# Performance work log

Hardware: AMD Instinct MI355X
Metric: run time of the kernel (lower is better)

The kernel has to match this reference:

```python
import jax, jax.numpy as jnp
import numpy as np

B, H, W, C = 2, 64, 64, 256
G, K, L = 16, 9, 2
Cg = C // G


def _ln(x, g, b, eps=1e-6):
    m = jnp.mean(x, -1, keepdims=True)
    v = jnp.mean((x - m) ** 2, -1, keepdims=True)
    return (x - m) * jax.lax.rsqrt(v + eps) * g + b


def _conv(x, w, b=None, groups=1):
    y = jax.lax.conv_general_dilated(x, w, (1, 1), 'SAME',
        dimension_numbers=('NHWC', 'HWIO', 'NHWC'), feature_group_count=groups)
    return y if b is None else y + b


def _gelu(x):
    return jax.nn.gelu(x, approximate=False)  # torch nn.GELU (exact erf)


def _dcnv3(x, dw_w, dw_b, dwn_g, dwn_b, off_w, off_b, msk_w, msk_b,
           inp_w, inp_b, out_w, out_b, offset_scale=1.0):
    # x: [B,H,W,C] channels-last. kernel=3, stride=1, pad=1, dilation=1.
    xp = x @ inp_w + inp_b                                   # input_proj
    f = _gelu(_ln(_conv(x, dw_w, dw_b, groups=C), dwn_g, dwn_b))  # dw_conv branch
    off = (f @ off_w + off_b).reshape(B, H, W, G, K, 2) * offset_scale  # pixel units (x,y)
    mask = jax.nn.softmax((f @ msk_w + msk_b).reshape(B, H, W, G, K), axis=-1)
    dy, dx = jnp.meshgrid(jnp.arange(3.0) - 1.0, jnp.arange(3.0) - 1.0, indexing='ij')
    gx = dx.reshape(-1)
    gy = dy.reshape(-1)  # [K] kernel dilation grid
    # sampling locations in the zero-padded (pad=1) frame; pixel i center = i+0.5
    loc_x = (jnp.arange(W, dtype=x.dtype) + 1.5)[None, None, :, None, None] + gx + off[..., 0]
    loc_y = (jnp.arange(H, dtype=x.dtype) + 1.5)[None, :, None, None, None] + gy + off[..., 1]
    xg = jnp.pad(xp, ((0, 0), (1, 1), (1, 1), (0, 0))).reshape(B, H + 2, W + 2, G, Cg)
    px = loc_x - 0.5
    py = loc_y - 0.5
    x0 = jnp.floor(px).astype(jnp.int32)
    y0 = jnp.floor(py).astype(jnp.int32)
    fx = (px - x0)[..., None]
    fy = (py - y0)[..., None]
    Hp, Wp = H + 2, W + 2
    bi = jnp.arange(B).reshape(B, 1, 1, 1, 1)
    gi = jnp.arange(G).reshape(1, 1, 1, G, 1)

    def gather(yi, xi):  # zero padding outside bounds (grid_sample padding_mode='zeros')
        ok = ((yi >= 0) & (yi < Hp) & (xi >= 0) & (xi < Wp)).astype(x.dtype)[..., None]
        return xg[bi, jnp.clip(yi, 0, Hp - 1), jnp.clip(xi, 0, Wp - 1), gi] * ok

    top = gather(y0, x0) * (1 - fx) + gather(y0, x0 + 1) * fx
    bot = gather(y0 + 1, x0) * (1 - fx) + gather(y0 + 1, x0 + 1) * fx
    samp = top * (1 - fy) + bot * fy                         # [B,H,W,G,K,Cg]
    out = (samp * mask[..., None]).sum(4).reshape(B, H, W, C)
    return out @ out_w + out_b                               # output_proj


def _leffn(x, dc_w, dc_b, g, b, c1_w, c1_b, c2_w, c2_b, gamma):
    y = _ln(_conv(x, dc_w, dc_b, groups=C), g, b)
    y = _gelu(y @ c1_w + c1_b) @ c2_w + c2_b
    return x + gamma * y


def _cbam(x, w1, w2, sa_w, g, b):
    fc = lambda v: jax.nn.relu(v @ w1) @ w2
    ca = jax.nn.sigmoid(fc(x.mean((1, 2))) + fc(x.max((1, 2))))[:, None, None, :]
    x = x * ca
    sm = jnp.stack([x.mean(-1), x.max(-1)], -1)              # [B,H,W,2]
    x = x * jax.nn.sigmoid(_conv(sm, sa_w))
    return _ln(x, g, b)


def _upsample(x, w, bb, g, bt):
    y = jax.image.resize(x, (B, 2 * H, 2 * W, C), 'bilinear')  # align_corners=False
    y = _conv(y, w, bb)                                        # 3x3, C -> C//2
    return _gelu(_ln(y, g, bt))


def _forward(x, ln1_g, ln1_b, dw_w, dw_b, dwn_g, dwn_b, off_w, off_b, msk_w, msk_b,
             inp_w, inp_b, out_w, out_b, ln2_g, ln2_b, dc_w, dc_b, fn_g, fn_b,
             c1_w, c1_b, c2_w, c2_b, ffn_gamma, ca_w1, ca_w2, sa_w, cb_g, cb_b,
             nf_g, nf_b, up_w, up_b, up_g, up_bt):
    x = _cbam(x, ca_w1, ca_w2, sa_w, cb_g, cb_b)
    for i in range(L):  # fixed small depth; structural loop
        x = x + _dcnv3(_ln(x, ln1_g[i], ln1_b[i]), dw_w[i], dw_b[i], dwn_g[i], dwn_b[i],
                       off_w[i], off_b[i], msk_w[i], msk_b[i], inp_w[i], inp_b[i],
                       out_w[i], out_b[i])
        x = x + _leffn(_ln(x, ln2_g[i], ln2_b[i]), dc_w[i], dc_b[i], fn_g[i], fn_b[i],
                       c1_w[i], c1_b[i], c2_w[i], c2_b[i], ffn_gamma[i])
    x = _ln(x, nf_g, nf_b)
    return _upsample(x, up_w, up_b, up_g, up_bt)


def setup_inputs() -> dict:
    ks = iter(jax.random.split(jax.random.key(0), 80))
    r = lambda shp, s=0.02: jax.random.normal(next(ks), shp, dtype=jnp.float32) * s
    one = lambda shp: jnp.ones(shp, jnp.float32)
    zero = lambda shp: jnp.zeros(shp, jnp.float32)
    return dict(
        x=jax.random.normal(next(ks), (B, H, W, C), dtype=jnp.float32),
        ln1_g=one((L, C)), ln1_b=zero((L, C)),
        dw_w=r((L, 3, 3, 1, C)), dw_b=zero((L, C)),
        dwn_g=one((L, C)), dwn_b=zero((L, C)),
        off_w=r((L, C, G * K * 2), 0.01), off_b=zero((L, G * K * 2)),
        msk_w=r((L, C, G * K)), msk_b=zero((L, G * K)),
        inp_w=r((L, C, C)), inp_b=zero((L, C)),
        out_w=r((L, C, C)), out_b=zero((L, C)),
        ln2_g=one((L, C)), ln2_b=zero((L, C)),
        dc_w=r((L, 7, 7, 1, C)), dc_b=zero((L, C)),
        fn_g=one((L, C)), fn_b=zero((L, C)),
        c1_w=r((L, C, 4 * C)), c1_b=zero((L, 4 * C)),
        c2_w=r((L, 4 * C, C)), c2_b=zero((L, C)),
        ffn_gamma=0.7 * one((L, C)),
        ca_w1=r((C, C // 16)), ca_w2=r((C // 16, C)),
        sa_w=r((7, 7, 2, 1)),
        cb_g=one((C,)), cb_b=zero((C,)),
        nf_g=one((C,)), nf_b=zero((C,)),
        up_w=r((3, 3, C, C // 2)), up_b=zero((C // 2,)),
        up_g=one((C // 2,)), up_bt=zero((C // 2,)),
    )


def reference(x, ln1_g, ln1_b, dw_w, dw_b, dwn_g, dwn_b, off_w, off_b, msk_w, msk_b,
              inp_w, inp_b, out_w, out_b, ln2_g, ln2_b, dc_w, dc_b, fn_g, fn_b,
              c1_w, c1_b, c2_w, c2_b, ffn_gamma, ca_w1, ca_w2, sa_w, cb_g, cb_b,
              nf_g, nf_b, up_w, up_b, up_g, up_bt):
    return _forward(x, ln1_g, ln1_b, dw_w, dw_b, dwn_g, dwn_b, off_w, off_b, msk_w, msk_b,
                    inp_w, inp_b, out_w, out_b, ln2_g, ln2_b, dc_w, dc_b, fn_g, fn_b,
                    c1_w, c1_b, c2_w, c2_b, ffn_gamma, ca_w1, ca_w2, sa_w, cb_g, cb_b,
                    nf_g, nf_b, up_w, up_b, up_g, up_bt)
```

## Files before the change

kernel.cpp:

```cpp
#include <hip/hip_runtime.h>
#include <math.h>

#define B_ 2
#define H_ 64
#define W_ 64
#define C_ 256
#define G_ 16
#define HW_ (H_*W_)
#define M_ (B_*HW_)
#define C4_ (4*C_)
#define OFFN_ 288
#define MSKN_ 144
#define OMN_ 432
#define UH_ 128
#define UW_ 128
#define MUP_ (B_*UH_*UW_)
#define KUP_ (9*C_)
#define NOUT_ 128

typedef short short8 __attribute__((ext_vector_type(8)));
typedef float f32x4 __attribute__((ext_vector_type(4)));
typedef unsigned short us4 __attribute__((ext_vector_type(4)));

__device__ __forceinline__ float gelu_f(float x){
  return 0.5f * x * (1.f + erff(x * 0.70710678118654752440f));
}
__device__ __forceinline__ float sigmoid_f(float x){ return 1.f/(1.f+expf(-x)); }
__device__ __forceinline__ unsigned short f2bf(float x){
  unsigned int u = __float_as_uint(x);
  unsigned int r = (u + 0x7fffu + ((u>>16)&1u)) >> 16;
  return (unsigned short)r;
}
__device__ __forceinline__ float bf2f(unsigned short u){
  return __uint_as_float(((unsigned int)u) << 16);
}
__device__ __forceinline__ float bfl(unsigned int u){ return __uint_as_float(u<<16); }
__device__ __forceinline__ float bfh(unsigned int u){ return __uint_as_float(u & 0xffff0000u); }
__device__ __forceinline__ unsigned int pk(float a, float b){
  return (unsigned int)f2bf(a) | ((unsigned int)f2bf(b) << 16);
}

__device__ __forceinline__ void block_sum2(float& s, float& ss, float* sm){
  #pragma unroll
  for (int off=32; off>0; off>>=1){ s += __shfl_down(s, off); ss += __shfl_down(ss, off); }
  int lane = threadIdx.x & 63, wid = threadIdx.x >> 6;
  if (lane == 0){ sm[wid] = s; sm[4+wid] = ss; }
  __syncthreads();
  float a = 0.f, b = 0.f;
  int nw = blockDim.x >> 6;
  for (int i=0;i<nw;i++){ a += sm[i]; b += sm[4+i]; }
  s = a; ss = b;
}

__device__ __forceinline__ void block_summax(float& s, float& m, float* sm){
  #pragma unroll
  for (int off=32; off>0; off>>=1){ s += __shfl_down(s, off); m = fmaxf(m, __shfl_down(m, off)); }
  int lane = threadIdx.x & 63, wid = threadIdx.x >> 6;
  if (lane == 0){ sm[wid] = s; sm[4+wid] = m; }
  __syncthreads();
  float a = 0.f, b = -3.4e38f;
  int nw = blockDim.x >> 6;
  for (int i=0;i<nw;i++){ a += sm[i]; b = fmaxf(b, sm[4+i]); }
  s = a; m = b;
}

#define NJOBS 13
struct WtJobs {
  const float* src[NJOBS];
  unsigned short* dst[NJOBS];
  int Kd[NJOBS], Nd[NJOBS];
  int tOff[NJOBS+1];
};

__global__ __launch_bounds__(256) void k_wt_all(WtJobs J){
  __shared__ float tile[32][33];
  int bid = blockIdx.x;
  int j = 0;
  while (bid >= J.tOff[j+1]) j++;
  int lt = bid - J.tOff[j];
  const float* W = J.src[j];
  unsigned short* Wt = J.dst[j];
  int Kd = J.Kd[j], Nd = J.Nd[j];
  int ktiles = Kd >> 5;
  int k0 = (lt % ktiles) * 32, n0 = (lt / ktiles) * 32;
  int t = threadIdx.x;
  int r = t>>3, c4 = (t&7)*4;
  float4 v = make_float4(0.f,0.f,0.f,0.f);
  if (n0 + c4 < Nd) v = *(const float4*)(W + (size_t)(k0+r)*Nd + n0 + c4);
  tile[c4+0][r]=v.x; tile[c4+1][r]=v.y; tile[c4+2][r]=v.z; tile[c4+3][r]=v.w;
  __syncthreads();
  if (n0 + r < Nd){
    us4 o;
    o.x = f2bf(tile[r][c4+0]); o.y = f2bf(tile[r][c4+1]);
    o.z = f2bf(tile[r][c4+2]); o.w = f2bf(tile[r][c4+3]);
    *(us4*)(Wt + (size_t)(n0+r)*Kd + k0 + c4) = o;
  }
}

__global__ __launch_bounds__(256) void k_chpool(const float* __restrict__ Xin,
      float* __restrict__ psum, float* __restrict__ pmax){
  int chunk = blockIdx.x, b = blockIdx.y; int c = threadIdx.x;
  const float* p = Xin + (((size_t)b*HW_) + chunk*32)*C_ + c;
  float s = 0.f, m = -3.4e38f;
  for (int i=0;i<32;i++){ float v = p[(size_t)i*C_]; s += v; m = fmaxf(m, v); }
  psum[(b*128+chunk)*C_+c] = s; pmax[(b*128+chunk)*C_+c] = m;
}

__global__ __launch_bounds__(512) void k_ca(const float* __restrict__ psum, const float* __restrict__ pmax,
    const float* __restrict__ w1, const float* __restrict__ w2, float* __restrict__ ca){
  __shared__ float pm[2][256], px[2][256], hh[2][2][16];
  int t = threadIdx.x;
  {
    int b = t >> 8, c = t & 255;
    float s = 0.f, m = -3.4e38f;
    for (int ch=0; ch<128; ch++){ s += psum[(b*128+ch)*256+c]; m = fmaxf(m, pmax[(b*128+ch)*256+c]); }
    pm[b][c] = s * (1.f/4096.f); px[b][c] = m;
  }
  __syncthreads();
  if (t < 64){
    int b = t >> 5, typ = (t >> 4) & 1, j = t & 15;
    const float* src = typ ? px[b] : pm[b];
    float a = 0.f;
    for (int c2=0;c2<256;c2++) a += src[c2]*w1[c2*16+j];
    hh[b][typ][j] = fmaxf(a, 0.f);
  }
  __syncthreads();
  {
    int b = t >> 8, c = t & 255;
    float a = 0.f;
    for (int j=0;j<16;j++) a += (hh[b][0][j]+hh[b][1][j]) * w2[j*256+c];
    ca[b*256+c] = sigmoid_f(a);
  }
}

__global__ __launch_bounds__(256) void k_apply_ca(const float* __restrict__ Xin, float* __restrict__ X,
    const float* __restrict__ ca, float* __restrict__ smean, float* __restrict__ smax){
  __shared__ float sm[12];
  int pix = blockIdx.x, c = threadIdx.x;
  int b = pix >> 12;
  float v = Xin[(size_t)pix*C_+c] * ca[b*C_+c];
  X[(size_t)pix*C_+c] = v;
  float s = v, m = v;
  block_summax(s, m, sm);
  if (c == 0){ smean[pix] = s * (1.f/C_); smax[pix] = m; }
}

__global__ __launch_bounds__(256) void k_sa(const float* __restrict__ smean, const float* __restrict__ smax,
    const float* __restrict__ w, float* __restrict__ sa){
  int pix = blockIdx.x*256 + threadIdx.x;
  if (pix >= M_) return;
  int b = pix >> 12, hw = pix & 4095, h = hw >> 6, ww = hw & 63;
  float s = 0.f;
  for (int ky=0;ky<7;ky++){
    int hh = h + ky - 3; if (hh < 0 || hh >= H_) continue;
    for (int kx=0;kx<7;kx++){
      int xx = ww + kx - 3; if (xx < 0 || xx >= W_) continue;
      int q = (b<<12) + (hh<<6) + xx;
      s += smean[q]*w[(ky*7+kx)*2+0] + smax[q]*w[(ky*7+kx)*2+1];
    }
  }
  sa[pix] = sigmoid_f(s);
}

__global__ __launch_bounds__(256) void k_mul_ln_ln1(float* __restrict__ X, const float* __restrict__ sa,
    const float* __restrict__ g, const float* __restrict__ b,
    const float* __restrict__ g1, const float* __restrict__ b1, unsigned short* __restrict__ Tb){
  __shared__ float sm[12];
  int pix = blockIdx.x, c = threadIdx.x;
  float v = X[(size_t)pix*C_+c] * sa[pix];
  float s = v, ss = v*v;
  block_sum2(s, ss, sm);
  float mean = s * (1.f/C_), var = ss*(1.f/C_) - mean*mean;
  float r = rsqrtf(var + 1e-6f);
  float x0 = (v-mean)*r*g[c] + b[c];
  X[(size_t)pix*C_+c] = x0;
  __syncthreads();
  s = x0; ss = x0*x0;
  block_sum2(s, ss, sm);
  mean = s * (1.f/C_); var = ss*(1.f/C_) - mean*mean;
  r = rsqrtf(var + 1e-6f);
  Tb[(size_t)pix*C_+c] = f2bf((x0-mean)*r*g1[c] + b1[c]);
}

template<int KS, int DOGELU>
__global__ __launch_bounds__(256) void k_dwconv(const unsigned short* __restrict__ T,
    unsigned short* __restrict__ Out,
    const float* __restrict__ w, const float* __restrict__ bias,
    const float* __restrict__ g, const float* __restrict__ bb){
  constexpr int R = KS/2;
  int t = blockIdx.x*256 + threadIdx.x;
  int pix = t >> 5, grp = t & 31;
  int c0 = grp*8;
  int b = pix >> 12, hw = pix & 4095, h = hw >> 6, ww = hw & 63;
  float acc[8];
  {
    float4 b0 = *(const float4*)(bias + c0), b1 = *(const float4*)(bias + c0 + 4);
    acc[0]=b0.x; acc[1]=b0.y; acc[2]=b0.z; acc[3]=b0.w;
    acc[4]=b1.x; acc[5]=b1.y; acc[6]=b1.z; acc[7]=b1.w;
  }
  const unsigned short* tb = T + ((size_t)b*HW_)*C_ + c0;
  for (int ky=0;ky<KS;ky++){
    int hh = h + ky - R; if (hh < 0 || hh >= H_) continue;
    for (int kx=0;kx<KS;kx++){
      int xx = ww + kx - R; if (xx < 0 || xx >= W_) continue;
      uint4 a = *(const uint4*)(tb + ((size_t)hh*W_+xx)*C_);
      const float* wp = w + (ky*KS+kx)*C_ + c0;
      float4 w0 = *(const float4*)wp, w1 = *(const float4*)(wp+4);
      acc[0] += bfl(a.x)*w0.x; acc[1] += bfh(a.x)*w0.y;
      acc[2] += bfl(a.y)*w0.z; acc[3] += bfh(a.y)*w0.w;
      acc[4] += bfl(a.z)*w1.x; acc[5] += bfh(a.z)*w1.y;
      acc[6] += bfl(a.w)*w1.z; acc[7] += bfh(a.w)*w1.w;
    }
  }
  float s = 0.f, ss = 0.f;
  #pragma unroll
  for (int i=0;i<8;i++){ s += acc[i]; ss += acc[i]*acc[i]; }
  #pragma unroll
  for (int off=1; off<32; off<<=1){ s += __shfl_xor(s, off); ss += __shfl_xor(ss, off); }
  float mean = s * (1.f/C_), var = ss*(1.f/C_) - mean*mean;
  float r = rsqrtf(var + 1e-6f);
  float4 g0 = *(const float4*)(g + c0), g1 = *(const float4*)(g + c0 + 4);
  float4 p0 = *(const float4*)(bb + c0), p1 = *(const float4*)(bb + c0 + 4);
  float o[8];
  o[0]=(acc[0]-mean)*r*g0.x+p0.x; o[1]=(acc[1]-mean)*r*g0.y+p0.y;
  o[2]=(acc[2]-mean)*r*g0.z+p0.z; o[3]=(acc[3]-mean)*r*g0.w+p0.w;
  o[4]=(acc[4]-mean)*r*g1.x+p1.x; o[5]=(acc[5]-mean)*r*g1.y+p1.y;
  o[6]=(acc[6]-mean)*r*g1.z+p1.z; o[7]=(acc[7]-mean)*r*g1.w+p1.w;
  if (DOGELU){
    #pragma unroll
    for (int i=0;i<8;i++) o[i] = gelu_f(o[i]);
  }
  uint4 ov;
  ov.x = pk(o[0],o[1]); ov.y = pk(o[2],o[3]); ov.z = pk(o[4],o[5]); ov.w = pk(o[6],o[7]);
  *(uint4*)(Out + (size_t)pix*C_ + c0) = ov;
}

template<int TM, int EP, int OUTBF>
__global__ __launch_bounds__(256) void k_gemm_mfma(
    const unsigned short* __restrict__ A, const unsigned short* __restrict__ Bt,
    void* __restrict__ OutV, const float* __restrict__ bias,
    const float* __restrict__ bias2, int Ni, int Ki)
{
  constexpr int LD = 40;
  __shared__ unsigned short As[TM*LD];
  __shared__ unsigned short Bs[128*LD];
  const int tid = threadIdx.x;
  const int wave = tid >> 6, lane = tid & 63;
  const int m0 = blockIdx.x * TM, n0 = blockIdx.y * 128;
  const int wm0 = (wave >> 1) * (TM/2);
  const int wn0 = (wave & 1) * 64;
  constexpr int MI = TM/32;
  f32x4 acc[MI][4] = {};
  const int lm = lane & 15, kq = lane >> 4;
  constexpr int ACH = TM*4/256;

  for (int k0 = 0; k0 < Ki; k0 += 32){
    #pragma unroll
    for (int i=0;i<ACH;i++){
      int ch = tid*ACH + i;
      int r = ch >> 2, cc = (ch & 3) << 3;
      short8 v = *(const short8*)(A + (size_t)(m0 + r)*Ki + k0 + cc);
      *(short8*)(As + r*LD + cc) = v;
    }
    #pragma unroll
    for (int i=0;i<2;i++){
      int ch = tid + 256*i;
      int r = ch >> 2, cc = (ch & 3) << 3;
      short8 v = {};
      if (n0 + r < Ni) v = *(const short8*)(Bt + (size_t)(n0 + r)*Ki + k0 + cc);
      *(short8*)(Bs + r*LD + cc) = v;
    }
    __syncthreads();
    short8 af[MI], bf[4];
    #pragma unroll
    for (int mi=0;mi<MI;mi++) af[mi] = *(const short8*)(As + (wm0 + mi*16 + lm)*LD + kq*8);
    #pragma unroll
    for (int ni=0;ni<4;ni++)  bf[ni] = *(const short8*)(Bs + (wn0 + ni*16 + lm)*LD + kq*8);
    #pragma unroll
    for (int mi=0;mi<MI;mi++)
      #pragma unroll
      for (int ni=0;ni<4;ni++)
        acc[mi][ni] = __builtin_amdgcn_mfma_f32_16x16x32_bf16(af[mi], bf[ni], acc[mi][ni], 0,0,0);
    __syncthreads();
  }
  #pragma unroll
  for (int mi=0;mi<MI;mi++){
    #pragma unroll
    for (int ni=0;ni<4;ni++){
      int n = n0 + wn0 + ni*16 + lm;
      if (n < Ni){
        float bv;
        if constexpr (EP==4) bv = (n < OFFN_) ? bias[n] : bias2[n-OFFN_];
        else bv = bias[n];
        #pragma unroll
        for (int r=0;r<4;r++){
          int m = m0 + wm0 + mi*16 + kq*4 + r;
          size_t o = (size_t)m*Ni + n;
          float v = acc[mi][ni][r] + bv;
          if constexpr (EP==1) v = gelu_f(v);
          if constexpr (OUTBF) ((unsigned short*)OutV)[o] = f2bf(v);
          else                 ((float*)OutV)[o] = v;
        }
      }
    }
  }
}

template<int EP>
__global__ __launch_bounds__(256) void k_gemm_ln(
    const unsigned short* __restrict__ A, const unsigned short* __restrict__ Bt,
    float* __restrict__ X, const float* __restrict__ bias,
    const unsigned short* __restrict__ res2b, const float* __restrict__ gamma,
    unsigned short* __restrict__ OutTb,
    const float* __restrict__ lng, const float* __restrict__ lnb, int Ki)
{
  constexpr int LD = 40;
  __shared__ unsigned short As[32*LD];
  __shared__ unsigned short Bs[256*LD];
  __shared__ float rs[32][2], rq[32][2];
  const int tid = threadIdx.x;
  const int wave = tid >> 6, lane = tid & 63;
  const int m0 = blockIdx.x * 32;
  const int wm0 = (wave >> 1) * 16;
  const int wn0 = (wave & 1) * 128;
  const int lm = lane & 15, kq = lane >> 4;
  f32x4 acc[8] = {};

  for (int k0 = 0; k0 < Ki; k0 += 32){
    if (tid < 128){
      int r = tid >> 2, cc = (tid & 3) << 3;
      short8 v = *(const short8*)(A + (size_t)(m0 + r)*Ki + k0 + cc);
      *(short8*)(As + r*LD + cc) = v;
    }
    #pragma unroll
    for (int i=0;i<4;i++){
      int ch = tid + 256*i;
      int r = ch >> 2, cc = (ch & 3) << 3;
      short8 v = *(const short8*)(Bt + (size_t)r*Ki + k0 + cc);
      *(short8*)(Bs + r*LD + cc) = v;
    }
    __syncthreads();
    short8 af = *(const short8*)(As + (wm0 + lm)*LD + kq*8);
    short8 bf[8];
    #pragma unroll
    for (int ni=0;ni<8;ni++) bf[ni] = *(const short8*)(Bs + (wn0 + ni*16 + lm)*LD + kq*8);
    #pragma unroll
    for (int ni=0;ni<8;ni++)
      acc[ni] = __builtin_amdgcn_mfma_f32_16x16x32_bf16(af, bf[ni], acc[ni], 0,0,0);
    __syncthreads();
  }
  int nn[8]; float bv[8], gv[8];
  #pragma unroll
  for (int ni=0;ni<8;ni++){
    nn[ni] = wn0 + ni*16 + lm;
    bv[ni] = bias[nn[ni]];
    if constexpr (EP==3) gv[ni] = gamma[nn[ni]];
  }
  float ps[4] = {}, pq[4] = {};
  #pragma unroll
  for (int r=0;r<4;r++){
    int m = m0 + wm0 + kq*4 + r;
    #pragma unroll
    for (int ni=0;ni<8;ni++){
      size_t o = (size_t)m*C_ + nn[ni];
      float v = acc[ni][r] + bv[ni];
      if constexpr (EP==2) v = X[o] + v;
      if constexpr (EP==3) v = X[o] + bf2f(res2b[o]) + gv[ni]*v;
      X[o] = v;
      acc[ni][r] = v;
      ps[r] += v; pq[r] += v*v;
    }
  }
  #pragma unroll
  for (int off=1; off<16; off<<=1){
    #pragma unroll
    for (int r=0;r<4;r++){ ps[r] += __shfl_xor(ps[r], off); pq[r] += __shfl_xor(pq[r], off); }
  }
  if (lm == 0){
    #pragma unroll
    for (int r=0;r<4;r++){
      rs[wm0 + kq*4 + r][wave & 1] = ps[r];
      rq[wm0 + kq*4 + r][wave & 1] = pq[r];
    }
  }
  __syncthreads();
  float lg[8], lb[8];
  #pragma unroll
  for (int ni=0;ni<8;ni++){ lg[ni] = lng[nn[ni]]; lb[ni] = lnb[nn[ni]]; }
  #pragma unroll
  for (int r=0;r<4;r++){
    int row = wm0 + kq*4 + r;
    int m = m0 + row;
    float s = rs[row][0] + rs[row][1];
    float q = rq[row][0] + rq[row][1];
    float mean = s * (1.f/C_), var = q*(1.f/C_) - mean*mean;
    float rstd = rsqrtf(var + 1e-6f);
    #pragma unroll
    for (int ni=0;ni<8;ni++){
      size_t o = (size_t)m*C_ + nn[ni];
      OutTb[o] = f2bf((acc[ni][r]-mean)*rstd*lg[ni] + lb[ni]);
    }
  }
}

__global__ __launch_bounds__(256) void k_dcn(const unsigned short* __restrict__ xp,
    const float* __restrict__ OM, unsigned short* __restrict__ S){
  __shared__ float lom[16*OMN_];
  int pix0 = blockIdx.x * 16;
  {
    const float* gsrc = OM + (size_t)pix0*OMN_;
    for (int idx = threadIdx.x; idx < 16*OMN_; idx += 256) lom[idx] = gsrc[idx];
  }
  __syncthreads();
  int pl = threadIdx.x >> 4, g = threadIdx.x & 15;
  int pix = pix0 + pl;
  int b = pix >> 12, hw = pix & 4095, h = hw >> 6, ww = hw & 63;
  const float* offp = lom + pl*OMN_ + g*18;
  const float* mp   = lom + pl*OMN_ + OFFN_ + g*9;
  const unsigned short* xpb = xp + ((size_t)b*HW_)*C_ + g*16;
  float e[9]; float mx = -3.4e38f;
  #pragma unroll
  for (int k=0;k<9;k++){ e[k] = mp[k]; mx = fmaxf(mx, e[k]); }
  float ssum = 0.f;
  #pragma unroll
  for (int k=0;k<9;k++){ e[k] = expf(e[k]-mx); ssum += e[k]; }
  float rinv = 1.f/ssum;
  float acc[16] = {};
  #pragma unroll
  for (int k=0;k<9;k++){
    float ox = offp[k*2+0], oy = offp[k*2+1];
    float px = (float)(ww + (k%3)) + ox;
    float py = (float)(h  + (k/3)) + oy;
    int x0 = (int)floorf(px), y0 = (int)floorf(py);
    float fx = px - (float)x0, fy = py - (float)y0;
    float mk = e[k]*rinv;
    float w00 = mk*(1.f-fx)*(1.f-fy), w01 = mk*fx*(1.f-fy);
    float w10 = mk*(1.f-fx)*fy,       w11 = mk*fx*fy;
    #define CORNER(yy,xx,WGT) do{ \
      if ((yy)>=1 && (yy)<=H_ && (xx)>=1 && (xx)<=W_){ \
        const unsigned short* p = xpb + ((size_t)((yy)-1)*W_ + ((xx)-1))*C_; \
        uint4 a0 = *(const uint4*)p; uint4 a1 = *(const uint4*)(p+8); \
        acc[0]+=WGT*bfl(a0.x); acc[1]+=WGT*bfh(a0.x); acc[2]+=WGT*bfl(a0.y); acc[3]+=WGT*bfh(a0.y); \
        acc[4]+=WGT*bfl(a0.z); acc[5]+=WGT*bfh(a0.z); acc[6]+=WGT*bfl(a0.w); acc[7]+=WGT*bfh(a0.w); \
        acc[8]+=WGT*bfl(a1.x); acc[9]+=WGT*bfh(a1.x); acc[10]+=WGT*bfl(a1.y); acc[11]+=WGT*bfh(a1.y); \
        acc[12]+=WGT*bfl(a1.z); acc[13]+=WGT*bfh(a1.z); acc[14]+=WGT*bfl(a1.w); acc[15]+=WGT*bfh(a1.w); \
      } \
    }while(0)
    CORNER(y0,   x0,   w00);
    CORNER(y0,   x0+1, w01);
    CORNER(y0+1, x0,   w10);
    CORNER(y0+1, x0+1, w11);
    #undef CORNER
  }
  unsigned short* sp = S + (size_t)pix*C_ + g*16;
  uint4 o0, o1;
  o0.x = pk(acc[0],acc[1]);   o0.y = pk(acc[2],acc[3]);
  o0.z = pk(acc[4],acc[5]);   o0.w = pk(acc[6],acc[7]);
  o1.x = pk(acc[8],acc[9]);   o1.y = pk(acc[10],acc[11]);
  o1.z = pk(acc[12],acc[13]); o1.w = pk(acc[14],acc[15]);
  *(uint4*)sp = o0;
  *(uint4*)(sp+8) = o1;
}

__global__ __launch_bounds__(256) void k_upsample(const unsigned short* __restrict__ T, unsigned short* __restrict__ U){
  int t = blockIdx.x*256 + threadIdx.x;
  int opix = t >> 5, grp = t & 31;
  int c0 = grp*8;
  int ox = opix & 127, oy = (opix >> 7) & 127, b = opix >> 14;
  float sy = oy*0.5f - 0.25f, sx = ox*0.5f - 0.25f;
  int y0 = (int)floorf(sy), x0 = (int)floorf(sx);
  float fy = sy - (float)y0, fx = sx - (float)x0;
  int y0c = min(max(y0,0),H_-1), y1c = min(max(y0+1,0),H_-1);
  int x0c = min(max(x0,0),W_-1), x1c = min(max(x0+1,0),W_-1);
  const unsigned short* tb = T + ((size_t)b*HW_)*C_ + c0;
  uint4 q00 = *(const uint4*)(tb + ((size_t)y0c*W_+x0c)*C_);
  uint4 q01 = *(const uint4*)(tb + ((size_t)y0c*W_+x1c)*C_);
  uint4 q10 = *(const uint4*)(tb + ((size_t)y1c*W_+x0c)*C_);
  uint4 q11 = *(const uint4*)(tb + ((size_t)y1c*W_+x1c)*C_);
  float w00=(1.f-fy)*(1.f-fx), w01=(1.f-fy)*fx, w10=fy*(1.f-fx), w11=fy*fx;
  float o[8];
  o[0]=w00*bfl(q00.x)+w01*bfl(q01.x)+w10*bfl(q10.x)+w11*bfl(q11.x);
  o[1]=w00*bfh(q00.x)+w01*bfh(q01.x)+w10*bfh(q10.x)+w11*bfh(q11.x);
  o[2]=w00*bfl(q00.y)+w01*bfl(q01.y)+w10*bfl(q10.y)+w11*bfl(q11.y);
  o[3]=w00*bfh(q00.y)+w01*bfh(q01.y)+w10*bfh(q10.y)+w11*bfh(q11.y);
  o[4]=w00*bfl(q00.z)+w01*bfl(q01.z)+w10*bfl(q10.z)+w11*bfl(q11.z);
  o[5]=w00*bfh(q00.z)+w01*bfh(q01.z)+w10*bfh(q10.z)+w11*bfh(q11.z);
  o[6]=w00*bfl(q00.w)+w01*bfl(q01.w)+w10*bfl(q10.w)+w11*bfl(q11.w);
  o[7]=w00*bfh(q00.w)+w01*bfh(q01.w)+w10*bfh(q10.w)+w11*bfh(q11.w);
  uint4 ov;
  ov.x = pk(o[0],o[1]); ov.y = pk(o[2],o[3]); ov.z = pk(o[4],o[5]); ov.w = pk(o[6],o[7]);
  *(uint4*)(U + (size_t)opix*C_ + c0) = ov;
}

__global__ __launch_bounds__(256) void k_upconv_ln(
    const unsigned short* __restrict__ U, const unsigned short* __restrict__ Wt,
    float* __restrict__ Out, const float* __restrict__ bias,
    const float* __restrict__ g, const float* __restrict__ bb)
{
  constexpr int LD = 72;
  __shared__ unsigned short As[64*LD];
  __shared__ unsigned short Bs[128*LD];
  __shared__ float rs[64][2], rq[64][2];
  const int tid = threadIdx.x;
  const int wave = tid >> 6, lane = tid & 63;
  const int m0 = blockIdx.x * 64;
  const int wm0 = (wave >> 1) * 32;
  const int wn0 = (wave & 1) * 64;
  const int lm = lane & 15, kq = lane >> 4;
  f32x4 acc[2][4] = {};
  const int r0 = tid >> 3, cA = (tid & 7) << 3;
  int bar[2], oyr[2], oxr[2];
  #pragma unroll
  for (int i=0;i<2;i++){
    int m = m0 + r0 + 32*i;
    bar[i] = m >> 14; oyr[i] = (m >> 7) & 127; oxr[i] = m & 127;
  }

  for (int k0 = 0; k0 < KUP_; k0 += 64){
    int tap = k0 >> 8, cc0 = k0 & 255;
    int dy = tap/3 - 1, dx = tap%3 - 1;
    #pragma unroll
    for (int i=0;i<2;i++){
      int iy = oyr[i] + dy, ix = oxr[i] + dx;
      short8 v = {};
      if (iy >= 0 && iy < UH_ && ix >= 0 && ix < UW_)
        v = *(const short8*)(U + (((size_t)bar[i]*UH_ + iy)*UW_ + ix)*C_ + cc0 + cA);
      *(short8*)(As + (r0 + 32*i)*LD + cA) = v;
    }
    #pragma unroll
    for (int i=0;i<4;i++){
      int r = r0 + 32*i;
      short8 v = *(const short8*)(Wt + (size_t)r*KUP_ + k0 + cA);
      *(short8*)(Bs + r*LD + cA) = v;
    }
    __syncthreads();
    short8 af[2][2], bf[4][2];
    #pragma unroll
    for (int mi=0;mi<2;mi++)
      #pragma unroll
      for (int kk=0;kk<2;kk++)
        af[mi][kk] = *(const short8*)(As + (wm0 + mi*16 + lm)*LD + kk*32 + kq*8);
    #pragma unroll
    for (int ni=0;ni<4;ni++)
      #pragma unroll
      for (int kk=0;kk<2;kk++)
        bf[ni][kk] = *(const short8*)(Bs + (wn0 + ni*16 + lm)*LD + kk*32 + kq*8);
    #pragma unroll
    for (int kk=0;kk<2;kk++)
      #pragma unroll
      for (int mi=0;mi<2;mi++)
        #pragma unroll
        for (int ni=0;ni<4;ni++)
          acc[mi][ni] = __builtin_amdgcn_mfma_f32_16x16x32_bf16(af[mi][kk], bf[ni][kk], acc[mi][ni], 0,0,0);
    __syncthreads();
  }
  int nn[4]; float bv[4];
  #pragma unroll
  for (int ni=0;ni<4;ni++){ nn[ni] = wn0 + ni*16 + lm; bv[ni] = bias[nn[ni]]; }
  float ps[2][4] = {}, pq[2][4] = {};
  #pragma unroll
  for (int mi=0;mi<2;mi++)
    #pragma unroll
    for (int r=0;r<4;r++)
      #pragma unroll
      for (int ni=0;ni<4;ni++){
        float v = acc[mi][ni][r] + bv[ni];
        acc[mi][ni][r] = v;
        ps[mi][r] += v; pq[mi][r] += v*v;
      }
  #pragma unroll
  for (int off=1; off<16; off<<=1){
    #pragma unroll
    for (int mi=0;mi<2;mi++)
      #pragma unroll
      for (int r=0;r<4;r++){ ps[mi][r] += __shfl_xor(ps[mi][r], off); pq[mi][r] += __shfl_xor(pq[mi][r], off); }
  }
  if (lm == 0){
    #pragma unroll
    for (int mi=0;mi<2;mi++)
      #pragma unroll
      for (int r=0;r<4;r++){
        rs[wm0 + mi*16 + kq*4 + r][wave & 1] = ps[mi][r];
        rq[wm0 + mi*16 + kq*4 + r][wave & 1] = pq[mi][r];
      }
  }
  __syncthreads();
  float gv[4], pv[4];
  #pragma unroll
  for (int ni=0;ni<4;ni++){ gv[ni] = g[nn[ni]]; pv[ni] = bb[nn[ni]]; }
  #pragma unroll
  for (int mi=0;mi<2;mi++)
    #pragma unroll
    for (int r=0;r<4;r++){
      int row = wm0 + mi*16 + kq*4 + r;
      int m = m0 + row;
      float s = rs[row][0] + rs[row][1];
      float q = rq[row][0] + rq[row][1];
      float mean = s * (1.f/NOUT_), var = q*(1.f/NOUT_) - mean*mean;
      float rstd = rsqrtf(var + 1e-6f);
      #pragma unroll
      for (int ni=0;ni<4;ni++)
        Out[(size_t)m*NOUT_ + nn[ni]] = gelu_f((acc[mi][ni][r]-mean)*rstd*gv[ni] + pv[ni]);
    }
}

extern "C" void kernel_launch(void* const* d_in, const int* in_sizes, int n_in,
                              void* d_out, int out_size, void* d_ws, size_t ws_size,
                              hipStream_t stream)
{
  (void)in_sizes; (void)n_in; (void)out_size; (void)ws_size;
  const float* x_in = (const float*)d_in[0];
  char* w = (char*)d_ws;
  const size_t MB = 1u<<20;
  float* X    = (float*)(w + 0*MB);
  float* OM   = (float*)(w + 8*MB);
  unsigned short* MIDb = (unsigned short*)(w + 22*MB);
  unsigned short* Ub   = MIDb;
  unsigned short* Tb   = (unsigned short*)(w + 38*MB);
  unsigned short* Fb   = (unsigned short*)(w + 42*MB);
  unsigned short* XPb  = (unsigned short*)(w + 46*MB);
  unsigned short* DW7b = (unsigned short*)(w + 50*MB);
  unsigned short* Sb   = (unsigned short*)(w + 54*MB);
  unsigned short* WT   = (unsigned short*)(w + 58*MB);
  float* psum = (float*)(w + 62*MB);
  float* pmax = psum + 65536;
  float* ca   = pmax + 65536;
  float* smean= ca + 512;
  float* smax = smean + 8192;
  float* sa   = smax + 8192;

  unsigned short* WtInp[2], *WtOut[2], *WtOM[2], *WtC1[2], *WtC2[2];
  {
    size_t o = 0;
    for (int i=0;i<2;i++){
      WtInp[i] = WT + o; o += 65536;
      WtOut[i] = WT + o; o += 65536;
      WtOM[i]  = WT + o; o += 110592;
      WtC1[i]  = WT + o; o += 262144;
      WtC2[i]  = WT + o; o += 262144;
    }
  }
  unsigned short* WtUp = WT + 1531904;

  WtJobs J;
  {
    int ji = 0, toff = 0;
    auto add = [&](const float* s, unsigned short* d, int Kd, int Nd){
      J.src[ji]=s; J.dst[ji]=d; J.Kd[ji]=Kd; J.Nd[ji]=Nd;
      J.tOff[ji]=toff; toff += (Kd>>5) * ((Nd+31)>>5); ji++;
    };
    for (int i=0;i<2;i++){
      add((const float*)d_in[11] + (size_t)i*C_*C_,   WtInp[i], C_, C_);
      add((const float*)d_in[13] + (size_t)i*C_*C_,   WtOut[i], C_, C_);
      add((const float*)d_in[7]  + (size_t)i*C_*OFFN_, WtOM[i], C_, OFFN_);
      add((const float*)d_in[9]  + (size_t)i*C_*MSKN_, WtOM[i] + (size_t)OFFN_*C_, C_, MSKN_);
      add((const float*)d_in[21] + (size_t)i*C_*C4_,  WtC1[i], C_, C4_);
      add((const float*)d_in[23] + (size_t)i*C4_*C_,  WtC2[i], C4_, C_);
    }
    add((const float*)d_in[33], WtUp, KUP_, NOUT_);
    J.tOff[ji] = toff;
    k_wt_all<<<toff,256,0,stream>>>(J);
  }

  k_chpool<<<dim3(128,2),256,0,stream>>>(x_in, psum, pmax);
  k_ca<<<1,512,0,stream>>>(psum, pmax, (const float*)d_in[26], (const float*)d_in[27], ca);
  k_apply_ca<<<M_,256,0,stream>>>(x_in, X, ca, smean, smax);
  k_sa<<<M_/256,256,0,stream>>>(smean, smax, (const float*)d_in[28], sa);
  k_mul_ln_ln1<<<M_,256,0,stream>>>(X, sa, (const float*)d_in[29], (const float*)d_in[30],
      (const float*)d_in[1], (const float*)d_in[2], Tb);

  for (int i=0;i<2;i++){
    const float* dww  = (const float*)d_in[3] + i*9*C_;
    const float* dwb  = (const float*)d_in[4] + i*C_;
    const float* dwng = (const float*)d_in[5] + i*C_;
    const float* dwnb = (const float*)d_in[6] + i*C_;
    const float* offb = (const float*)d_in[8] + i*OFFN_;
    const float* mskb = (const float*)d_in[10] + i*MSKN_;
    const float* inpb = (const float*)d_in[12] + i*C_;
    const float* outb = (const float*)d_in[14] + i*C_;
    const float* ln2g = (const float*)d_in[15] + i*C_;
    const float* ln2b = (const float*)d_in[16] + i*C_;
    const float* dcw  = (const float*)d_in[17] + i*49*C_;
    const float* dcb  = (const float*)d_in[18] + i*C_;
    const float* fng  = (const float*)d_in[19] + i*C_;
    const float* fnb  = (const float*)d_in[20] + i*C_;
    const float* c1b  = (const float*)d_in[22] + i*C4_;
    const float* c2b  = (const float*)d_in[24] + i*C_;
    const float* gam  = (const float*)d_in[25] + i*C_;
    const float* nxg = (i==0) ? (const float*)d_in[1] + C_ : (const float*)d_in[31];
    const float* nxb = (i==0) ? (const float*)d_in[2] + C_ : (const float*)d_in[32];

    k_gemm_mfma<64,0,1><<<dim3(M_/64,2),256,0,stream>>>(Tb, WtInp[i], XPb, inpb, nullptr, C_, C_);
    k_dwconv<3,1><<<M_*32/256,256,0,stream>>>(Tb, Fb, dww, dwb, dwng, dwnb);
    k_gemm_mfma<64,4,0><<<dim3(M_/64,4),256,0,stream>>>(Fb, WtOM[i], OM, offb, mskb, OMN_, C_);
    k_dcn<<<M_/16,256,0,stream>>>(XPb, OM, Sb);
    k_gemm_ln<2><<<M_/32,256,0,stream>>>(Sb, WtOut[i], X, outb, nullptr, nullptr, Tb, ln2g, ln2b, C_);

    k_dwconv<7,0><<<M_*32/256,256,0,stream>>>(Tb, DW7b, dcw, dcb, fng, fnb);
    k_gemm_mfma<128,1,1><<<dim3(M_/128,8),256,0,stream>>>(DW7b, WtC1[i], MIDb, c1b, nullptr, C4_, C_);
    k_gemm_ln<3><<<M_/32,256,0,stream>>>(MIDb, WtC2[i], X, c2b, Tb, gam, Tb, nxg, nxb, C4_);
  }

  k_upsample<<<MUP_*32/256,256,0,stream>>>(Tb, Ub);
  k_upconv_ln<<<MUP_/64,256,0,stream>>>(Ub, WtUp, (float*)d_out, (const float*)d_in[34],
      (const float*)d_in[35], (const float*)d_in[36]);
}
```

Measured before the change: 520.5 us.

## Register-block dwconv over 4-pixel strips and deepen GEMM K tiles to 64/128

The depthwise conv kernel now computes four horizontally adjacent pixels per thread. Each loaded input column is reused across up to four taps, and each row's weights are loaded into registers once, which cuts redundant global loads. The MFMA GEMMs, the LN-fused GEMM and the upconv GEMM take larger K steps per shared-memory stage (64 or 128), halving the barrier and load-loop iterations. The input-projection and offset/mask GEMMs also switch to 32-row tiles to launch more blocks. The cost is more registers per thread, which may lower occupancy, and larger LDS tiles.

```diff
diff --git a/kernel.cpp b/kernel.cpp
--- a/kernel.cpp
+++ b/kernel.cpp
@@ -188,60 +188,90 @@
     const float* __restrict__ w, const float* __restrict__ bias,
     const float* __restrict__ g, const float* __restrict__ bb){
   constexpr int R = KS/2;
+  constexpr int NC = KS + 3;
   int t = blockIdx.x*256 + threadIdx.x;
-  int pix = t >> 5, grp = t & 31;
+  int strip = t >> 5, grp = t & 31;
   int c0 = grp*8;
-  int b = pix >> 12, hw = pix & 4095, h = hw >> 6, ww = hw & 63;
-  float acc[8];
+  int b = strip >> 10, rem = strip & 1023, h = rem >> 4, w4 = (rem & 15) << 2;
+  float acc[4][8];
   {
     float4 b0 = *(const float4*)(bias + c0), b1 = *(const float4*)(bias + c0 + 4);
-    acc[0]=b0.x; acc[1]=b0.y; acc[2]=b0.z; acc[3]=b0.w;
-    acc[4]=b1.x; acc[5]=b1.y; acc[6]=b1.z; acc[7]=b1.w;
+    #pragma unroll
+    for (int px=0;px<4;px++){
+      acc[px][0]=b0.x; acc[px][1]=b0.y; acc[px][2]=b0.z; acc[px][3]=b0.w;
+      acc[px][4]=b1.x; acc[px][5]=b1.y; acc[px][6]=b1.z; acc[px][7]=b1.w;
+    }
   }
   const unsigned short* tb = T + ((size_t)b*HW_)*C_ + c0;
   for (int ky=0;ky<KS;ky++){
-    int hh = h + ky - R; if (hh < 0 || hh >= H_) continue;
+    int iy = h + ky - R; if (iy < 0 || iy >= H_) continue;
+    float wr[KS][8];
+    #pragma unroll
     for (int kx=0;kx<KS;kx++){
-      int xx = ww + kx - R; if (xx < 0 || xx >= W_) continue;
-      uint4 a = *(const uint4*)(tb + ((size_t)hh*W_+xx)*C_);
       const float* wp = w + (ky*KS+kx)*C_ + c0;
       float4 w0 = *(const float4*)wp, w1 = *(const float4*)(wp+4);
-      acc[0] += bfl(a.x)*w0.x; acc[1] += bfh(a.x)*w0.y;
-      acc[2] += bfl(a.y)*w0.z; acc[3] += bfh(a.y)*w0.w;
-      acc[4] += bfl(a.z)*w1.x; acc[5] += bfh(a.z)*w1.y;
-      acc[6] += bfl(a.w)*w1.z; acc[7] += bfh(a.w)*w1.w;
-    }
-  }
-  float s = 0.f, ss = 0.f;
-  #pragma unroll
-  for (int i=0;i<8;i++){ s += acc[i]; ss += acc[i]*acc[i]; }
-  #pragma unroll
-  for (int off=1; off<32; off<<=1){ s += __shfl_xor(s, off); ss += __shfl_xor(ss, off); }
-  float mean = s * (1.f/C_), var = ss*(1.f/C_) - mean*mean;
-  float r = rsqrtf(var + 1e-6f);
+      wr[kx][0]=w0.x; wr[kx][1]=w0.y; wr[kx][2]=w0.z; wr[kx][3]=w0.w;
+      wr[kx][4]=w1.x; wr[kx][5]=w1.y; wr[kx][6]=w1.z; wr[kx][7]=w1.w;
+    }
+    #pragma unroll
+    for (int ixr=0;ixr<NC;ixr++){
+      int ix = w4 + ixr - R; if (ix < 0 || ix >= W_) continue;
+      uint4 a = *(const uint4*)(tb + ((size_t)iy*W_+ix)*C_);
+      float t8[8] = {bfl(a.x),bfh(a.x),bfl(a.y),bfh(a.y),bfl(a.z),bfh(a.z),bfl(a.w),bfh(a.w)};
+      #pragma unroll
+      for (int px=0;px<4;px++){
+        constexpr int dummy = 0; (void)dummy;
+        int kx = ixr - px;
+        if (kx >= 0 && kx < KS){
+          #pragma unroll
+          for (int c=0;c<8;c++) acc[px][c] += t8[c]*wr[ixr-px][c];
+        }
+      }
+    }
+  }
+  float s[4], q[4];
+  #pragma unroll
+  for (int px=0;px<4;px++){
+    float a = 0.f, b2 = 0.f;
+    #pragma unroll
+    for (int c=0;c<8;c++){ a += acc[px][c]; b2 += acc[px][c]*acc[px][c]; }
+    s[px] = a; q[px] = b2;
+  }
+  #pragma unroll
+  for (int off=1; off<32; off<<=1){
+    #pragma unroll
+    for (int px=0;px<4;px++){ s[px] += __shfl_xor(s[px], off); q[px] += __shfl_xor(q[px], off); }
+  }
   float4 g0 = *(const float4*)(g + c0), g1 = *(const float4*)(g + c0 + 4);
   float4 p0 = *(const float4*)(bb + c0), p1 = *(const float4*)(bb + c0 + 4);
-  float o[8];
-  o[0]=(acc[0]-mean)*r*g0.x+p0.x; o[1]=(acc[1]-mean)*r*g0.y+p0.y;
-  o[2]=(acc[2]-mean)*r*g0.z+p0.z; o[3]=(acc[3]-mean)*r*g0.w+p0.w;
-  o[4]=(acc[4]-mean)*r*g1.x+p1.x; o[5]=(acc[5]-mean)*r*g1.y+p1.y;
-  o[6]=(acc[6]-mean)*r*g1.z+p1.z; o[7]=(acc[7]-mean)*r*g1.w+p1.w;
-  if (DOGELU){
-    #pragma unroll
-    for (int i=0;i<8;i++) o[i] = gelu_f(o[i]);
-  }
-  uint4 ov;
-  ov.x = pk(o[0],o[1]); ov.y = pk(o[2],o[3]); ov.z = pk(o[4],o[5]); ov.w = pk(o[6],o[7]);
-  *(uint4*)(Out + (size_t)pix*C_ + c0) = ov;
-}
-
-template<int TM, int EP, int OUTBF>
+  float gg[8] = {g0.x,g0.y,g0.z,g0.w,g1.x,g1.y,g1.z,g1.w};
+  float pp[8] = {p0.x,p0.y,p0.z,p0.w,p1.x,p1.y,p1.z,p1.w};
+  #pragma unroll
+  for (int px=0;px<4;px++){
+    float mean = s[px] * (1.f/C_), var = q[px]*(1.f/C_) - mean*mean;
+    float r = rsqrtf(var + 1e-6f);
+    float o[8];
+    #pragma unroll
+    for (int c=0;c<8;c++){
+      float v = (acc[px][c]-mean)*r*gg[c] + pp[c];
+      o[c] = DOGELU ? gelu_f(v) : v;
+    }
+    uint4 ov;
+    ov.x = pk(o[0],o[1]); ov.y = pk(o[2],o[3]); ov.z = pk(o[4],o[5]); ov.w = pk(o[6],o[7]);
+    size_t pix = ((size_t)b*H_ + h)*W_ + w4 + px;
+    *(uint4*)(Out + pix*C_ + c0) = ov;
+  }
+}
+
+template<int TM, int BK, int EP, int OUTBF>
 __global__ __launch_bounds__(256) void k_gemm_mfma(
     const unsigned short* __restrict__ A, const unsigned short* __restrict__ Bt,
     void* __restrict__ OutV, const float* __restrict__ bias,
     const float* __restrict__ bias2, int Ni, int Ki)
 {
-  constexpr int LD = 40;
+  constexpr int LD = BK + 8;
+  constexpr int CH = BK/8;
+  constexpr int KI = BK/32;
   __shared__ unsigned short As[TM*LD];
   __shared__ unsigned short Bs[128*LD];
   const int tid = threadIdx.x;
@@ -249,38 +279,41 @@
   const int m0 = blockIdx.x * TM, n0 = blockIdx.y * 128;
   const int wm0 = (wave >> 1) * (TM/2);
   const int wn0 = (wave & 1) * 64;
-  constexpr int MI = TM/32;
+  constexpr int MI = (TM+31)/32;
   f32x4 acc[MI][4] = {};
   const int lm = lane & 15, kq = lane >> 4;
-  constexpr int ACH = TM*4/256;
-
-  for (int k0 = 0; k0 < Ki; k0 += 32){
-    #pragma unroll
-    for (int i=0;i<ACH;i++){
-      int ch = tid*ACH + i;
-      int r = ch >> 2, cc = (ch & 3) << 3;
+
+  for (int k0 = 0; k0 < Ki; k0 += BK){
+    for (int ch = tid; ch < TM*CH; ch += 256){
+      int r = ch / CH, cc = (ch % CH) << 3;
       short8 v = *(const short8*)(A + (size_t)(m0 + r)*Ki + k0 + cc);
       *(short8*)(As + r*LD + cc) = v;
     }
-    #pragma unroll
-    for (int i=0;i<2;i++){
-      int ch = tid + 256*i;
-      int r = ch >> 2, cc = (ch & 3) << 3;
+    for (int ch = tid; ch < 128*CH; ch += 256){
+      int r = ch / CH, cc = (ch % CH) << 3;
       short8 v = {};
       if (n0 + r < Ni) v = *(const short8*)(Bt + (size_t)(n0 + r)*Ki + k0 + cc);
       *(short8*)(Bs + r*LD + cc) = v;
     }
     __syncthreads();
-    short8 af[MI], bf[4];
-    #pragma unroll
-    for (int mi=0;mi<MI;mi++) af[mi] = *(const short8*)(As + (wm0 + mi*16 + lm)*LD + kq*8);
-    #pragma unroll
-    for (int ni=0;ni<4;ni++)  bf[ni] = *(const short8*)(Bs + (wn0 + ni*16 + lm)*LD + kq*8);
+    short8 af[MI][KI], bf4[4][KI];
     #pragma unroll
     for (int mi=0;mi<MI;mi++)
       #pragma unroll
-      for (int ni=0;ni<4;ni++)
-        acc[mi][ni] = __builtin_amdgcn_mfma_f32_16x16x32_bf16(af[mi], bf[ni], acc[mi][ni], 0,0,0);
+      for (int kk=0;kk<KI;kk++)
+        af[mi][kk] = *(const short8*)(As + (wm0 + mi*16 + lm)*LD + kk*32 + kq*8);
+    #pragma unroll
+    for (int ni=0;ni<4;ni++)
+      #pragma unroll
+      for (int kk=0;kk<KI;kk++)
+        bf4[ni][kk] = *(const short8*)(Bs + (wn0 + ni*16 + lm)*LD + kk*32 + kq*8);
+    #pragma unroll
+    for (int kk=0;kk<KI;kk++)
+      #pragma unroll
+      for (int mi=0;mi<MI;mi++)
+        #pragma unroll
+        for (int ni=0;ni<4;ni++)
+          acc[mi][ni] = __builtin_amdgcn_mfma_f32_16x16x32_bf16(af[mi][kk], bf4[ni][kk], acc[mi][ni], 0,0,0);
     __syncthreads();
   }
   #pragma unroll
@@ -314,7 +347,7 @@
     unsigned short* __restrict__ OutTb,
     const float* __restrict__ lng, const float* __restrict__ lnb, int Ki)
 {
-  constexpr int LD = 40;
+  constexpr int LD = 72;
   __shared__ unsigned short As[32*LD];
   __shared__ unsigned short Bs[256*LD];
   __shared__ float rs[32][2], rq[32][2];
@@ -326,27 +359,34 @@
   const int lm = lane & 15, kq = lane >> 4;
   f32x4 acc[8] = {};
 
-  for (int k0 = 0; k0 < Ki; k0 += 32){
-    if (tid < 128){
-      int r = tid >> 2, cc = (tid & 3) << 3;
+  for (int k0 = 0; k0 < Ki; k0 += 64){
+    {
+      int r = tid >> 3, cc = (tid & 7) << 3;
       short8 v = *(const short8*)(A + (size_t)(m0 + r)*Ki + k0 + cc);
       *(short8*)(As + r*LD + cc) = v;
     }
     #pragma unroll
-    for (int i=0;i<4;i++){
+    for (int i=0;i<8;i++){
       int ch = tid + 256*i;
-      int r = ch >> 2, cc = (ch & 3) << 3;
+      int r = ch >> 3, cc = (ch & 7) << 3;
       short8 v = *(const short8*)(Bt + (size_t)r*Ki + k0 + cc);
       *(short8*)(Bs + r*LD + cc) = v;
     }
     __syncthreads();
-    short8 af = *(const short8*)(As + (wm0 + lm)*LD + kq*8);
-    short8 bf[8];
-    #pragma unroll
-    for (int ni=0;ni<8;ni++) bf[ni] = *(const short8*)(Bs + (wn0 + ni*16 + lm)*LD + kq*8);
+    short8 af[2], bf4[8][2];
+    #pragma unroll
+    for (int kk=0;kk<2;kk++)
+      af[kk] = *(const short8*)(As + (wm0 + lm)*LD + kk*32 + kq*8);
     #pragma unroll
     for (int ni=0;ni<8;ni++)
-      acc[ni] = __builtin_amdgcn_mfma_f32_16x16x32_bf16(af, bf[ni], acc[ni], 0,0,0);
+      #pragma unroll
+      for (int kk=0;kk<2;kk++)
+        bf4[ni][kk] = *(const short8*)(Bs + (wn0 + ni*16 + lm)*LD + kk*32 + kq*8);
+    #pragma unroll
+    for (int kk=0;kk<2;kk++)
+      #pragma unroll
+      for (int ni=0;ni<8;ni++)
+        acc[ni] = __builtin_amdgcn_mfma_f32_16x16x32_bf16(af[kk], bf4[ni][kk], acc[ni], 0,0,0);
     __syncthreads();
   }
   int nn[8]; float bv[8], gv[8];
@@ -497,7 +537,7 @@
     float* __restrict__ Out, const float* __restrict__ bias,
     const float* __restrict__ g, const float* __restrict__ bb)
 {
-  constexpr int LD = 72;
+  constexpr int LD = 136;
   __shared__ unsigned short As[64*LD];
   __shared__ unsigned short Bs[128*LD];
   __shared__ float rs[64][2], rq[64][2];
@@ -508,50 +548,50 @@
   const int wn0 = (wave & 1) * 64;
   const int lm = lane & 15, kq = lane >> 4;
   f32x4 acc[2][4] = {};
-  const int r0 = tid >> 3, cA = (tid & 7) << 3;
-  int bar[2], oyr[2], oxr[2];
-  #pragma unroll
-  for (int i=0;i<2;i++){
-    int m = m0 + r0 + 32*i;
-    bar[i] = m >> 14; oyr[i] = (m >> 7) & 127; oxr[i] = m & 127;
-  }
-
-  for (int k0 = 0; k0 < KUP_; k0 += 64){
+  const int r0 = tid >> 2, cA0 = (tid & 3) << 5;
+  const int ma = m0 + r0;
+  const int ba = ma >> 14, oya = (ma >> 7) & 127, oxa = ma & 127;
+
+  for (int k0 = 0; k0 < KUP_; k0 += 128){
     int tap = k0 >> 8, cc0 = k0 & 255;
     int dy = tap/3 - 1, dx = tap%3 - 1;
-    #pragma unroll
-    for (int i=0;i<2;i++){
-      int iy = oyr[i] + dy, ix = oxr[i] + dx;
-      short8 v = {};
-      if (iy >= 0 && iy < UH_ && ix >= 0 && ix < UW_)
-        v = *(const short8*)(U + (((size_t)bar[i]*UH_ + iy)*UW_ + ix)*C_ + cc0 + cA);
-      *(short8*)(As + (r0 + 32*i)*LD + cA) = v;
-    }
-    #pragma unroll
-    for (int i=0;i<4;i++){
-      int r = r0 + 32*i;
-      short8 v = *(const short8*)(Wt + (size_t)r*KUP_ + k0 + cA);
-      *(short8*)(Bs + r*LD + cA) = v;
+    {
+      int iy = oya + dy, ix = oxa + dx;
+      bool ok = (iy >= 0 && iy < UH_ && ix >= 0 && ix < UW_);
+      const unsigned short* src = U + (((size_t)ba*UH_ + iy)*UW_ + ix)*C_ + cc0 + cA0;
+      #pragma unroll
+      for (int i=0;i<4;i++){
+        short8 v = {};
+        if (ok) v = *(const short8*)(src + i*8);
+        *(short8*)(As + r0*LD + cA0 + i*8) = v;
+      }
+    }
+    #pragma unroll
+    for (int i=0;i<8;i++){
+      int ch = tid + 256*i;
+      int r = ch >> 4, cc = (ch & 15) << 3;
+      short8 v = *(const short8*)(Wt + (size_t)r*KUP_ + k0 + cc);
+      *(short8*)(Bs + r*LD + cc) = v;
     }
     __syncthreads();
-    short8 af[2][2], bf[4][2];
+    short8 af[2][4], bf4[4][4];
     #pragma unroll
     for (int mi=0;mi<2;mi++)
       #pragma unroll
-      for (int kk=0;kk<2;kk++)
+      for (int kk=0;kk<4;kk++)
         af[mi][kk] = *(const short8*)(As + (wm0 + mi*16 + lm)*LD + kk*32 + kq*8);
     #pragma unroll
     for (int ni=0;ni<4;ni++)
       #pragma unroll
-      for (int kk=0;kk<2;kk++)
-        bf[ni][kk] = *(const short8*)(Bs + (wn0 + ni*16 + lm)*LD + kk*32 + kq*8);
-    #pragma unroll
-    for (int kk=0;kk<2;kk++)
+      for (int kk=0;kk<4;kk++)
+        bf4[ni][kk] = *(const short8*)(Bs + (wn0 + ni*16 + lm)*LD + kk*32 + kq*8);
+    #pragma unroll
+    for (int kk=0;kk<4;kk++)
       #pragma unroll
       for (int mi=0;mi<2;mi++)
         #pragma unroll
         for (int ni=0;ni<4;ni++)
-          acc[mi][ni] = __builtin_amdgcn_mfma_f32_16x16x32_bf16(af[mi][kk], bf[ni][kk], acc[mi][ni], 0,0,0);
+          acc[mi][ni] = __builtin_amdgcn_mfma_f32_16x16x32_bf16(af[mi][kk], bf4[ni][kk], acc[mi][ni], 0,0,0);
     __syncthreads();
   }
   int nn[4]; float bv[4];
@@ -690,14 +730,14 @@
     const float* nxg = (i==0) ? (const float*)d_in[1] + C_ : (const float*)d_in[31];
     const float* nxb = (i==0) ? (const float*)d_in[2] + C_ : (const float*)d_in[32];
 
-    k_gemm_mfma<64,0,1><<<dim3(M_/64,2),256,0,stream>>>(Tb, WtInp[i], XPb, inpb, nullptr, C_, C_);
-    k_dwconv<3,1><<<M_*32/256,256,0,stream>>>(Tb, Fb, dww, dwb, dwng, dwnb);
-    k_gemm_mfma<64,4,0><<<dim3(M_/64,4),256,0,stream>>>(Fb, WtOM[i], OM, offb, mskb, OMN_, C_);
+    k_gemm_mfma<32,64,0,1><<<dim3(M_/32,2),256,0,stream>>>(Tb, WtInp[i], XPb, inpb, nullptr, C_, C_);
+    k_dwconv<3,1><<<M_*32/(4*256),256,0,stream>>>(Tb, Fb, dww, dwb, dwng, dwnb);
+    k_gemm_mfma<32,64,4,0><<<dim3(M_/32,4),256,0,stream>>>(Fb, WtOM[i], OM, offb, mskb, OMN_, C_);
     k_dcn<<<M_/16,256,0,stream>>>(XPb, OM, Sb);
     k_gemm_ln<2><<<M_/32,256,0,stream>>>(Sb, WtOut[i], X, outb, nullptr, nullptr, Tb, ln2g, ln2b, C_);
 
-    k_dwconv<7,0><<<M_*32/256,256,0,stream>>>(Tb, DW7b, dcw, dcb, fng, fnb);
-    k_gemm_mfma<128,1,1><<<dim3(M_/128,8),256,0,stream>>>(DW7b, WtC1[i], MIDb, c1b, nullptr, C4_, C_);
+    k_dwconv<7,0><<<M_*32/(4*256),256,0,stream>>>(Tb, DW7b, dcw, dcb, fng, fnb);
+    k_gemm_mfma<128,64,1,1><<<dim3(M_/128,8),256,0,stream>>>(DW7b, WtC1[i], MIDb, c1b, nullptr, C4_, C_);
     k_gemm_ln<3><<<M_/32,256,0,stream>>>(MIDb, WtC2[i], X, c2b, Tb, gam, Tb, nxg, nxb, C4_);
   }
 
```

Measured after the change: 528.8 us. About the same (+1.6%).
